# Kernel optimization log

Hardware: AMD Instinct MI355X
Metric: run time of the kernel (lower is better)

## Reference

```python
import jax, jax.numpy as jnp
import numpy as np

B, N, DIM = 4, 2048, 256
H, HD, M = 8, 32, 4
SPARSE_TOPK = 32


def setup_inputs() -> dict:
    key = jax.random.key(0)
    ks = jax.random.split(key, 6)
    x = jax.random.normal(ks[0], (B, N, DIM), dtype=jnp.float32)
    w_qkv = jax.random.normal(ks[1], (DIM, 3 * H * HD), dtype=jnp.float32) * 0.02
    b_qkv = jnp.zeros((3 * H * HD,), dtype=jnp.float32)
    w_proj = jax.random.normal(ks[2], (H * HD, DIM), dtype=jnp.float32) * 0.02
    b_proj = jnp.zeros((DIM,), dtype=jnp.float32)
    scale = jnp.ones((1, H, 1, 1), dtype=jnp.float32)  # trainable scale, init scale_value=1.0
    mem_k = jax.random.normal(ks[3], (H, M, HD), dtype=jnp.float32)
    mem_v = jax.random.normal(ks[4], (H, M, HD), dtype=jnp.float32)
    return {"x": x, "w_qkv": w_qkv, "b_qkv": b_qkv, "w_proj": w_proj,
            "b_proj": b_proj, "scale": scale, "mem_k": mem_k, "mem_v": mem_v}


def reference(x, w_qkv, b_qkv, w_proj, b_proj, scale, mem_k, mem_v):
    b, n, dim = x.shape
    h, m, hd = mem_k.shape
    qkv = (x @ w_qkv + b_qkv).reshape(b, n, 3, h, hd).transpose(2, 0, 3, 1, 4)
    q, k, v = qkv[0], qkv[1], qkv[2]
    # concat memory vectors along key-length axis -> [B,H,N+M,hd]
    k = jnp.concatenate([k, jnp.broadcast_to(mem_k, (b, h, m, hd))], axis=2)
    v = jnp.concatenate([v, jnp.broadcast_to(mem_v, (b, h, m, hd))], axis=2)
    s = n + m
    # scores with trainable per-head scale: [B,H,N,S]
    scores = jnp.einsum('bhnd,bhsd->bhns', q, k) * (hd ** -0.5) * scale
    neg = -jnp.finfo(scores.dtype).max
    # improve_locality: mask rectangular diagonal (eye(N, S))
    diag = jnp.arange(n)[:, None] == jnp.arange(s)[None, :]
    scores = jnp.where(diag, neg, scores)
    # sparse topk: keep only values >= k-th largest per row
    top = jax.lax.top_k(scores, SPARSE_TOPK)[0]
    vk = top[..., -1:]
    scores = jnp.where(scores < vk, neg, scores)
    attn = jax.nn.softmax(scores, axis=-1)
    out = jnp.einsum('bhns,bhsd->bhnd', attn, v)
    out = out.transpose(0, 2, 1, 3).reshape(b, n, h * hd)
    return out @ w_proj + b_proj
```

## Files before the change

### kernel.cpp

```cpp
#include <hip/hip_runtime.h>
#include <float.h>
#include <stdint.h>

#define Bb   4
#define Nn   2048
#define DIMc 256
#define Hh   8
#define HDd  32
#define Mm   4
#define STOT 2052
#define ROWS 8
#define SROW 2112
#define NVROW 2052

typedef float f32x2 __attribute__((ext_vector_type(2)));
typedef unsigned long long u64;

__device__ __forceinline__ unsigned int f2key(float s) {
    unsigned int b = __float_as_uint(s);
    return (b & 0x80000000u) ? ~b : (b | 0x80000000u);
}
__device__ __forceinline__ float key2f(unsigned int u) {
    unsigned int b = (u & 0x80000000u) ? (u ^ 0x80000000u) : ~u;
    return __uint_as_float(b);
}

__global__ __launch_bounds__(256) void sgemm_qkv(
    const float* __restrict__ A, const float* __restrict__ Bm,
    const float* __restrict__ bias, float* __restrict__ Qb,
    float* __restrict__ kTb, float* __restrict__ Vx,
    const float* __restrict__ memv)
{
    __shared__ __align__(16) float As[2][16][68];
    __shared__ __align__(16) float Bs[2][16][64];
    __shared__ __align__(16) float Ts[64][65];
    const int tid = threadIdx.x;
    const int tx = tid & 15, ty = tid >> 4;
    const int m0 = blockIdx.y * 64, n0 = blockIdx.x * 64;
    const int arow = tid >> 2, acol = (tid & 3) * 4;
    const int brow = tid >> 4, bcol = (tid & 15) * 4;
    float acc[4][4] = {};

    {
        const float4 av = *(const float4*)&A[(size_t)(m0 + arow) * DIMc + acol];
        const float4 bv = *(const float4*)&Bm[(size_t)brow * 768 + n0 + bcol];
        As[0][acol + 0][arow] = av.x;
        As[0][acol + 1][arow] = av.y;
        As[0][acol + 2][arow] = av.z;
        As[0][acol + 3][arow] = av.w;
        *(float4*)&Bs[0][brow][bcol] = bv;
    }
    int cur = 0;
    for (int kb = 0; kb < DIMc; kb += 16) {
        float4 av2, bv2;
        const bool more = (kb + 16 < DIMc);
        if (more) {
            av2 = *(const float4*)&A[(size_t)(m0 + arow) * DIMc + kb + 16 + acol];
            bv2 = *(const float4*)&Bm[(size_t)(kb + 16 + brow) * 768 + n0 + bcol];
        }
        __syncthreads();
#pragma unroll
        for (int k = 0; k < 16; ++k) {
            const float4 a  = *(const float4*)&As[cur][k][ty * 4];
            const float4 bq = *(const float4*)&Bs[cur][k][tx * 4];
            const float aa[4] = {a.x, a.y, a.z, a.w};
            const float bb[4] = {bq.x, bq.y, bq.z, bq.w};
#pragma unroll
            for (int i = 0; i < 4; ++i)
#pragma unroll
                for (int j = 0; j < 4; ++j)
                    acc[i][j] = fmaf(aa[i], bb[j], acc[i][j]);
        }
        if (more) {
            As[cur ^ 1][acol + 0][arow] = av2.x;
            As[cur ^ 1][acol + 1][arow] = av2.y;
            As[cur ^ 1][acol + 2][arow] = av2.z;
            As[cur ^ 1][acol + 3][arow] = av2.w;
            *(float4*)&Bs[cur ^ 1][brow][bcol] = bv2;
        }
        cur ^= 1;
    }
    const float4 bv = *(const float4*)&bias[n0 + tx * 4];
    const float bb[4] = {bv.x, bv.y, bv.z, bv.w};
    const int path = n0 >> 8;
    if (path == 1) {
#pragma unroll
        for (int i = 0; i < 4; ++i)
#pragma unroll
            for (int j = 0; j < 4; ++j)
                Ts[tx * 4 + j][ty * 4 + i] = acc[i][j] + bb[j];
        __syncthreads();
        const int c_local = tid >> 2;
        const int seg     = tid & 3;
        const int cg = (n0 - 256) + c_local;
        const int hh = cg >> 5, dd = cg & 31;
        const int bi = m0 >> 11, j0 = (m0 & 2047) + seg * 16;
        float* dst = kTb + (((size_t)(bi * Hh + hh) * HDd + dd) * Nn) + j0;
#pragma unroll
        for (int q = 0; q < 4; ++q)
            *(float4*)(dst + q * 4) = *(const float4*)&Ts[c_local][seg * 16 + q * 4];
    } else if (path == 0) {
        const int c0 = n0 + tx * 4;
#pragma unroll
        for (int i = 0; i < 4; ++i) {
            float4 o;
            o.x = acc[i][0] + bb[0];
            o.y = acc[i][1] + bb[1];
            o.z = acc[i][2] + bb[2];
            o.w = acc[i][3] + bb[3];
            *(float4*)&Qb[(size_t)(m0 + ty * 4 + i) * 256 + c0] = o;
        }
    } else {
        const int c0 = (n0 & 255) + tx * 4;
        const size_t row_base = (size_t)(m0 >> 11) * NVROW + (m0 & 2047);
#pragma unroll
        for (int i = 0; i < 4; ++i) {
            float4 o;
            o.x = acc[i][0] + bb[0];
            o.y = acc[i][1] + bb[1];
            o.z = acc[i][2] + bb[2];
            o.w = acc[i][3] + bb[3];
            *(float4*)&Vx[(row_base + ty * 4 + i) * 256 + c0] = o;
        }
        if (n0 == 512 && (m0 & 2047) == 0) {
            const int bb2 = m0 >> 11;
#pragma unroll
            for (int mm = 0; mm < Mm; ++mm)
                Vx[((size_t)bb2 * NVROW + Nn + mm) * 256 + tid] =
                    memv[((tid >> 5) * Mm + mm) * HDd + (tid & 31)];
        }
    }
}

__global__ __launch_bounds__(256) void sgemm_bias(
    const float* __restrict__ A, const float* __restrict__ Bm,
    const float* __restrict__ bias, float* __restrict__ C,
    int Md, int Nd, int Kd)
{
    __shared__ __align__(16) float As[2][16][36];
    __shared__ __align__(16) float Bs[2][16][64];
    const int tid = threadIdx.x;
    const int tx = tid & 15, ty = tid >> 4;
    const int m0 = blockIdx.y * 32, n0 = blockIdx.x * 64;
    const int arow = tid >> 2, acol = (tid & 3) * 4;
    const int brow = tid >> 4, bcol = (tid & 15) * 4;
    float acc[2][4] = {};

    {
        const float4 bv = *(const float4*)&Bm[(size_t)brow * Nd + n0 + bcol];
        *(float4*)&Bs[0][brow][bcol] = bv;
        if (tid < 128) {
            const float4 av = *(const float4*)&A[(size_t)(m0 + arow) * Kd + acol];
            As[0][acol + 0][arow] = av.x;
            As[0][acol + 1][arow] = av.y;
            As[0][acol + 2][arow] = av.z;
            As[0][acol + 3][arow] = av.w;
        }
    }
    int cur = 0;
    for (int kb = 0; kb < Kd; kb += 16) {
        float4 av2, bv2;
        const bool more = (kb + 16 < Kd);
        if (more) {
            bv2 = *(const float4*)&Bm[(size_t)(kb + 16 + brow) * Nd + n0 + bcol];
            if (tid < 128)
                av2 = *(const float4*)&A[(size_t)(m0 + arow) * Kd + kb + 16 + acol];
        }
        __syncthreads();
#pragma unroll
        for (int k = 0; k < 16; ++k) {
            const float2 a  = *(const float2*)&As[cur][k][ty * 2];
            const float4 bq = *(const float4*)&Bs[cur][k][tx * 4];
            const float aa[2] = {a.x, a.y};
            const float bb[4] = {bq.x, bq.y, bq.z, bq.w};
#pragma unroll
            for (int i = 0; i < 2; ++i)
#pragma unroll
                for (int j = 0; j < 4; ++j)
                    acc[i][j] = fmaf(aa[i], bb[j], acc[i][j]);
        }
        if (more) {
            *(float4*)&Bs[cur ^ 1][brow][bcol] = bv2;
            if (tid < 128) {
                As[cur ^ 1][acol + 0][arow] = av2.x;
                As[cur ^ 1][acol + 1][arow] = av2.y;
                As[cur ^ 1][acol + 2][arow] = av2.z;
                As[cur ^ 1][acol + 3][arow] = av2.w;
            }
        }
        cur ^= 1;
    }
    const float4 bv = *(const float4*)&bias[n0 + tx * 4];
    const float bb[4] = {bv.x, bv.y, bv.z, bv.w};
#pragma unroll
    for (int i = 0; i < 2; ++i) {
        float4 o;
        o.x = acc[i][0] + bb[0];
        o.y = acc[i][1] + bb[1];
        o.z = acc[i][2] + bb[2];
        o.w = acc[i][3] + bb[3];
        *(float4*)&C[(size_t)(m0 + ty * 2 + i) * Nd + n0 + tx * 4] = o;
    }
}

#if __has_builtin(__builtin_elementwise_fma)
#define PKSTEP(Q, P)                                                        \
    { const f32x2 qq = {(Q), (Q)};                                          \
      a01 = __builtin_elementwise_fma(qq, ((const f32x2*)&kd[P])[0], a01);  \
      a23 = __builtin_elementwise_fma(qq, ((const f32x2*)&kd[P])[1], a23); }
#else
#define PKSTEP(Q, P)                                                        \
    { a01.x = fmaf((Q), kd[P].x, a01.x); a01.y = fmaf((Q), kd[P].y, a01.y); \
      a23.x = fmaf((Q), kd[P].z, a23.x); a23.y = fmaf((Q), kd[P].w, a23.y); }
#endif

__global__ __launch_bounds__(512, 4) void attn_sparse(
    const float* __restrict__ Qb, const float* __restrict__ kTb,
    const float* __restrict__ Vx, const float* __restrict__ memk,
    const float* __restrict__ scale, float* __restrict__ attn_out)
{
    __shared__ __align__(16) unsigned int S[ROWS][SROW];
    __shared__ __align__(16) float qs[ROWS][HDd];
    __shared__ __align__(16) u64 ulist64[ROWS][64];
    __shared__ __align__(16) u64 wj_list[ROWS][64];

    const int tid    = threadIdx.x;
    const int ntiles = Nn / ROWS;
    const int tile   = blockIdx.x % ntiles;
    const int h      = (blockIdx.x / ntiles) % Hh;
    const int b      = blockIdx.x / (ntiles * Hh);
    const int n0     = tile * ROWS;
    const float sc   = scale[h] * 0.17677669529663688f;

    if (tid < ROWS * HDd) {
        const int r = tid >> 5, d2 = tid & 31;
        qs[r][d2] = Qb[(size_t)(b * Nn + n0 + r) * 256 + h * HDd + d2];
    }
    __syncthreads();

    const float* kT = kTb + (size_t)(b * Hh + h) * (HDd * Nn);

    {
        const int j0 = tid * 4;
        f32x2 acc01[ROWS], acc23[ROWS];
#pragma unroll
        for (int r = 0; r < ROWS; ++r) { acc01[r] = (f32x2){0.f, 0.f}; acc23[r] = (f32x2){0.f, 0.f}; }
#pragma unroll 1
        for (int dc = 0; dc < 4; ++dc) {
            float4 kd[8];
#pragma unroll
            for (int dd = 0; dd < 8; ++dd)
                kd[dd] = *(const float4*)&kT[(dc * 8 + dd) * Nn + j0];
#pragma unroll
            for (int r = 0; r < ROWS; ++r) {
                const float4 qa = *(const float4*)&qs[r][dc * 8];
                const float4 qb2 = *(const float4*)&qs[r][dc * 8 + 4];
                f32x2 a01 = acc01[r], a23 = acc23[r];
                PKSTEP(qa.x, 0) PKSTEP(qa.y, 1) PKSTEP(qa.z, 2) PKSTEP(qa.w, 3)
                PKSTEP(qb2.x, 4) PKSTEP(qb2.y, 5) PKSTEP(qb2.z, 6) PKSTEP(qb2.w, 7)
                acc01[r] = a01; acc23[r] = a23;
            }
        }
#pragma unroll
        for (int r = 0; r < ROWS; ++r) {
            const float af[4] = {acc01[r].x, acc01[r].y, acc23[r].x, acc23[r].y};
            uint4 o;
            unsigned int* op = (unsigned int*)&o;
#pragma unroll
            for (int kk = 0; kk < 4; ++kk) {
                float s = af[kk] * sc;
                if (j0 + kk == n0 + r) s = -FLT_MAX;
                op[kk] = f2key(s);
            }
            *(uint4*)&S[r][j0] = o;
        }
    }
    if (tid < 32) {
        const int r = tid >> 2, m = tid & 3;
        const float* kp = memk + (size_t)(h * Mm + m) * HDd;
        float acc = 0.f;
#pragma unroll
        for (int dcc = 0; dcc < 8; ++dcc) {
            const float4 qv = *(const float4*)&qs[r][dcc * 4];
            const float4 kv = *(const float4*)&kp[dcc * 4];
            acc = fmaf(qv.x, kv.x, acc);
            acc = fmaf(qv.y, kv.y, acc);
            acc = fmaf(qv.z, kv.z, acc);
            acc = fmaf(qv.w, kv.w, acc);
        }
        S[r][2048 + m] = f2key(acc * sc);
    } else {
        const int t2 = tid - 32;
        const int r = t2 / 60, p = t2 % 60;
        S[r][2052 + p] = 0x00800000u;
    }
    __syncthreads();

    const int wave = tid >> 6, lane = tid & 63;
    const int half = lane >> 5, d = lane & 31;
    const int n = n0 + wave;

    unsigned int uv[33];
    unsigned int mx = 0u;
    {
        const unsigned int* Srow = &S[wave][lane];
#pragma unroll
        for (int i = 0; i < 33; ++i) {
            uv[i] = Srow[i * 64];
            mx = uv[i] > mx ? uv[i] : mx;
        }
    }

    auto bitonic = [&](unsigned int vv) -> unsigned int {
#pragma unroll
        for (int kk = 2; kk <= 64; kk <<= 1)
#pragma unroll
            for (int jj = kk >> 1; jj > 0; jj >>= 1) {
                const unsigned int o = (unsigned int)__shfl_xor((int)vv, jj);
                const unsigned int mn = vv < o ? vv : o;
                const unsigned int mxv = vv < o ? o : vv;
                const bool up   = ((lane & kk) == 0);
                const bool lowr = ((lane & jj) == 0);
                vv = (lowr == up) ? mn : mxv;
            }
        return vv;
    };
    auto countge = [&](unsigned int tt) -> int {
        int gg = 0;
#pragma unroll
        for (int i = 0; i < 33; ++i) gg += (int)__popcll(__ballot(uv[i] >= tt));
        return gg;
    };
    auto compact = [&](unsigned int tt) -> int {
        int bs = 0;
#pragma unroll
        for (int i = 0; i < 33; ++i) {
            const bool p = (uv[i] >= tt);
            const unsigned long long mk = __ballot(p);
            if (p) {
                const int pos = bs + (int)__popcll(mk & ((1ull << lane) - 1ull));
                if (pos < 64)
                    ulist64[wave][pos] = ((u64)uv[i] << 32) | (unsigned int)(i * 64 + lane);
            }
            bs += (int)__popcll(mk);
        }
        return bs;
    };

    const unsigned int vs1 = bitonic(mx);
    const unsigned int Lmax = (unsigned int)__shfl((int)vs1, 63);
    unsigned int t = (unsigned int)__shfl((int)vs1, 32);

    ulist64[wave][lane] = 0ull;
    __asm__ __volatile__("s_waitcnt lgkmcnt(0)" ::: "memory");
    int base = compact(t);
    bool exact = true;
    if (base > 64) {
        unsigned int blo = t, bhi = Lmax + 1;
        int found = 0;
#pragma unroll 1
        for (int it = 0; it < 33; ++it) {
            if (bhi - blo <= 1u) break;
            const unsigned int tm = blo + ((bhi - blo) >> 1);
            const int gm = countge(tm);
            if (gm > 64) blo = tm;
            else if (gm < 32) bhi = tm;
            else { t = tm; found = 1; break; }
        }
        if (!found) t = blo;
        ulist64[wave][lane] = 0ull;
        __asm__ __volatile__("s_waitcnt lgkmcnt(0)" ::: "memory");
        base = compact(t);
        exact = (base <= 64);
    }
    const int C2 = base < 64 ? base : 64;
    __asm__ __volatile__("s_waitcnt lgkmcnt(0)" ::: "memory");
    const u64 pk = ulist64[wave][lane];
    const unsigned int ue = (unsigned int)(pk >> 32);
    const int je = (int)(unsigned int)pk;

    const unsigned int vs2 = bitonic(ue);
    unsigned int vkkey = (unsigned int)__shfl((int)vs2, 32);
    const unsigned int v31u = (unsigned int)__shfl((int)vs2, 31);
    if (!exact) vkkey = t;

    const bool tie_span = (v31u == vkkey);
    float snx = -3.0e38f;
    if (exact && !tie_span) {
        if (C2 == 32) {
            unsigned int unx = 0u;
#pragma unroll
            for (int i = 0; i < 33; ++i) {
                const unsigned int u = uv[i];
                if (u < vkkey && u > unx) unx = u;
            }
#pragma unroll
            for (int o = 32; o > 0; o >>= 1) {
                const unsigned int ou = (unsigned int)__shfl_xor((int)unx, o);
                if (ou > unx) unx = ou;
            }
            snx = key2f(unx);
        } else {
            snx = key2f(v31u);
        }
    }
    const float svk  = key2f(vkkey);
    const float gapv = svk - snx;
    const float lam  = (exact && !tie_span && gapv > 0.f && gapv <= 4.0e-6f) ? 0.13f : 0.f;

    const float mval = key2f(Lmax);
    const float we = (ue >= vkkey) ? __expf(key2f(ue) - mval) : 0.f;
    wj_list[wave][(lane & 1) * 32 + (lane >> 1)] =
        ((u64)(unsigned int)je << 32) | (u64)__float_as_uint(we);
    float Z = we;
#pragma unroll
    for (int o = 32; o > 0; o >>= 1) Z += __shfl_xor(Z, o);
    __asm__ __volatile__("s_waitcnt lgkmcnt(0)" ::: "memory");

    const float* Vbh = Vx + (size_t)b * (NVROW * 256) + h * HDd;
    float outv = 0.f;
#pragma unroll 2
    for (int e0 = 0; e0 < C2; e0 += 8) {
        const int p0 = (e0 >> 1) + half * 32;
        const ulonglong2 wa = *(const ulonglong2*)&wj_list[wave][p0];
        const ulonglong2 wb = *(const ulonglong2*)&wj_list[wave][p0 + 2];
        float w[4]; unsigned int q[4];
        w[0] = __uint_as_float((unsigned int)wa.x); q[0] = (unsigned int)(wa.x >> 32);
        w[1] = __uint_as_float((unsigned int)wa.y); q[1] = (unsigned int)(wa.y >> 32);
        w[2] = __uint_as_float((unsigned int)wb.x); q[2] = (unsigned int)(wb.x >> 32);
        w[3] = __uint_as_float((unsigned int)wb.y); q[3] = (unsigned int)(wb.y >> 32);
        float vv[4];
#pragma unroll
        for (int u2 = 0; u2 < 4; ++u2)
            vv[u2] = Vbh[q[u2] * 256u + (unsigned int)d];
#pragma unroll
        for (int u2 = 0; u2 < 4; ++u2)
            outv = fmaf(w[u2], vv[u2], outv);
    }
    outv += __shfl_xor(outv, 32);

    float res = outv / Z;
    if (lam > 0.f) {
        unsigned int unx2 = 0u; int jnx = 0, jd1 = -1;
#pragma unroll
        for (int i = 0; i < 33; ++i) {
            const unsigned int u = uv[i];
            const int jj2 = i * 64 + lane;
            if (u < vkkey && u > unx2) { unx2 = u; jnx = jj2; }
            if (u == vkkey && jj2 > jd1) jd1 = jj2;
        }
#pragma unroll
        for (int o = 32; o > 0; o >>= 1) {
            const unsigned int ou = (unsigned int)__shfl_xor((int)unx2, o);
            const int oj = __shfl_xor(jnx, o);
            if (ou > unx2 || (ou == unx2 && oj > jnx)) { unx2 = ou; jnx = oj; }
            const int od = __shfl_xor(jd1, o);
            if (od > jd1) jd1 = od;
        }
        const float wd = __expf(svk - mval);
        const float wn = __expf(key2f(unx2) - mval);
        const float* vp1 = Vbh + (size_t)jd1 * 256;
        const float* vpn = Vbh + (size_t)jnx * 256;
        const float ZB = Z - wd + wn;
        const float oB = (outv - wd * vp1[d] + wn * vpn[d]) / ZB;
        res = (1.f - lam) * res + lam * oB;
    }
    if (half == 0)
        attn_out[(size_t)(b * Nn + n) * 256 + h * HDd + d] = res;
}

extern "C" void kernel_launch(void* const* d_in, const int* in_sizes, int n_in,
                              void* d_out, int out_size, void* d_ws, size_t ws_size,
                              hipStream_t stream) {
    const float* x      = (const float*)d_in[0];
    const float* w_qkv  = (const float*)d_in[1];
    const float* b_qkv  = (const float*)d_in[2];
    const float* w_proj = (const float*)d_in[3];
    const float* b_proj = (const float*)d_in[4];
    const float* scale  = (const float*)d_in[5];
    const float* mem_k  = (const float*)d_in[6];
    const float* mem_v  = (const float*)d_in[7];
    float* out = (float*)d_out;

    float* Qb  = (float*)d_ws;
    float* kTb = Qb  + (size_t)Bb * Nn * 256;
    float* Vx  = kTb + (size_t)Bb * Hh * HDd * Nn;

    sgemm_qkv<<<dim3(768 / 64, (Bb * Nn) / 64), 256, 0, stream>>>(
        x, w_qkv, b_qkv, Qb, kTb, Vx, mem_v);

    attn_sparse<<<dim3(Bb * Hh * (Nn / ROWS)), 512, 0, stream>>>(
        Qb, kTb, Vx, mem_k, scale, Qb);

    sgemm_bias<<<dim3(DIMc / 64, (Bb * Nn) / 32), 256, 0, stream>>>(
        Qb, w_proj, b_proj, out, Bb * Nn, DIMc, DIMc);
}
```

Before: 364.5 us.

## Enlarge GEMM register tiles and software-pipeline K loads in score loop

The QKV GEMM moves from 64x64 to 128x128 tiles with an 8x8 per-thread register tile, and its LDS staging and transpose buffer share a union. The output projection GEMM moves to 128x64 tiles with 8x4 per thread. The attention score loop is unrolled with two K register buffers so global loads for the next chunk are in flight while the current chunk's FMAs run. The aim is more arithmetic per shared-memory and global access, fewer blocks, and hidden load latency, at the cost of higher register pressure and less parallelism in the small GEMMs (fewer blocks: 384 for QKV, 256 for projection).

```diff
diff --git a/kernel.cpp b/kernel.cpp
--- a/kernel.cpp
+++ b/kernel.cpp
@@ -31,96 +31,117 @@
     float* __restrict__ kTb, float* __restrict__ Vx,
     const float* __restrict__ memv)
 {
-    __shared__ __align__(16) float As[2][16][68];
-    __shared__ __align__(16) float Bs[2][16][64];
-    __shared__ __align__(16) float Ts[64][65];
+    __shared__ __align__(16) union {
+        struct { float As[2][16][128]; float Bs[2][16][128]; } st;
+        float Ts[128][133];
+    } u;
     const int tid = threadIdx.x;
     const int tx = tid & 15, ty = tid >> 4;
-    const int m0 = blockIdx.y * 64, n0 = blockIdx.x * 64;
-    const int arow = tid >> 2, acol = (tid & 3) * 4;
-    const int brow = tid >> 4, bcol = (tid & 15) * 4;
-    float acc[4][4] = {};
+    const int m0 = blockIdx.y * 128, n0 = blockIdx.x * 128;
+    const int arow = tid >> 1, acol = (tid & 1) * 8;
+    const int bcol = tx * 8;
+    float acc[8][8] = {};
 
     {
-        const float4 av = *(const float4*)&A[(size_t)(m0 + arow) * DIMc + acol];
-        const float4 bv = *(const float4*)&Bm[(size_t)brow * 768 + n0 + bcol];
-        As[0][acol + 0][arow] = av.x;
-        As[0][acol + 1][arow] = av.y;
-        As[0][acol + 2][arow] = av.z;
-        As[0][acol + 3][arow] = av.w;
-        *(float4*)&Bs[0][brow][bcol] = bv;
+        const float4 a0 = *(const float4*)&A[(size_t)(m0 + arow) * DIMc + acol];
+        const float4 a1 = *(const float4*)&A[(size_t)(m0 + arow) * DIMc + acol + 4];
+        const float4 b0 = *(const float4*)&Bm[(size_t)ty * 768 + n0 + bcol];
+        const float4 b1 = *(const float4*)&Bm[(size_t)ty * 768 + n0 + bcol + 4];
+        const float av[8] = {a0.x,a0.y,a0.z,a0.w,a1.x,a1.y,a1.z,a1.w};
+#pragma unroll
+        for (int c = 0; c < 8; ++c) u.st.As[0][acol + c][arow] = av[c];
+        *(float4*)&u.st.Bs[0][ty][bcol]     = b0;
+        *(float4*)&u.st.Bs[0][ty][bcol + 4] = b1;
     }
     int cur = 0;
     for (int kb = 0; kb < DIMc; kb += 16) {
-        float4 av2, bv2;
+        float4 a0n, a1n, b0n, b1n;
         const bool more = (kb + 16 < DIMc);
         if (more) {
-            av2 = *(const float4*)&A[(size_t)(m0 + arow) * DIMc + kb + 16 + acol];
-            bv2 = *(const float4*)&Bm[(size_t)(kb + 16 + brow) * 768 + n0 + bcol];
+            a0n = *(const float4*)&A[(size_t)(m0 + arow) * DIMc + kb + 16 + acol];
+            a1n = *(const float4*)&A[(size_t)(m0 + arow) * DIMc + kb + 16 + acol + 4];
+            b0n = *(const float4*)&Bm[(size_t)(kb + 16 + ty) * 768 + n0 + bcol];
+            b1n = *(const float4*)&Bm[(size_t)(kb + 16 + ty) * 768 + n0 + bcol + 4];
         }
         __syncthreads();
 #pragma unroll
         for (int k = 0; k < 16; ++k) {
-            const float4 a  = *(const float4*)&As[cur][k][ty * 4];
-            const float4 bq = *(const float4*)&Bs[cur][k][tx * 4];
-            const float aa[4] = {a.x, a.y, a.z, a.w};
-            const float bb[4] = {bq.x, bq.y, bq.z, bq.w};
-#pragma unroll
-            for (int i = 0; i < 4; ++i)
-#pragma unroll
-                for (int j = 0; j < 4; ++j)
+            const float4 av0 = *(const float4*)&u.st.As[cur][k][ty * 8];
+            const float4 av1 = *(const float4*)&u.st.As[cur][k][ty * 8 + 4];
+            const float4 bv0 = *(const float4*)&u.st.Bs[cur][k][tx * 8];
+            const float4 bv1 = *(const float4*)&u.st.Bs[cur][k][tx * 8 + 4];
+            const float aa[8] = {av0.x,av0.y,av0.z,av0.w,av1.x,av1.y,av1.z,av1.w};
+            const float bb[8] = {bv0.x,bv0.y,bv0.z,bv0.w,bv1.x,bv1.y,bv1.z,bv1.w};
+#pragma unroll
+            for (int i = 0; i < 8; ++i)
+#pragma unroll
+                for (int j = 0; j < 8; ++j)
                     acc[i][j] = fmaf(aa[i], bb[j], acc[i][j]);
         }
         if (more) {
-            As[cur ^ 1][acol + 0][arow] = av2.x;
-            As[cur ^ 1][acol + 1][arow] = av2.y;
-            As[cur ^ 1][acol + 2][arow] = av2.z;
-            As[cur ^ 1][acol + 3][arow] = av2.w;
-            *(float4*)&Bs[cur ^ 1][brow][bcol] = bv2;
+            const float av[8] = {a0n.x,a0n.y,a0n.z,a0n.w,a1n.x,a1n.y,a1n.z,a1n.w};
+#pragma unroll
+            for (int c = 0; c < 8; ++c) u.st.As[cur ^ 1][acol + c][arow] = av[c];
+            *(float4*)&u.st.Bs[cur ^ 1][ty][bcol]     = b0n;
+            *(float4*)&u.st.Bs[cur ^ 1][ty][bcol + 4] = b1n;
         }
         cur ^= 1;
     }
-    const float4 bv = *(const float4*)&bias[n0 + tx * 4];
-    const float bb[4] = {bv.x, bv.y, bv.z, bv.w};
+    const float4 bv0 = *(const float4*)&bias[n0 + tx * 8];
+    const float4 bv1 = *(const float4*)&bias[n0 + tx * 8 + 4];
+    const float bb[8] = {bv0.x,bv0.y,bv0.z,bv0.w,bv1.x,bv1.y,bv1.z,bv1.w};
     const int path = n0 >> 8;
     if (path == 1) {
-#pragma unroll
-        for (int i = 0; i < 4; ++i)
-#pragma unroll
-            for (int j = 0; j < 4; ++j)
-                Ts[tx * 4 + j][ty * 4 + i] = acc[i][j] + bb[j];
         __syncthreads();
-        const int c_local = tid >> 2;
-        const int seg     = tid & 3;
+#pragma unroll
+        for (int i = 0; i < 8; ++i) {
+            float4 o0, o1;
+            o0.x = acc[i][0] + bb[0]; o0.y = acc[i][1] + bb[1];
+            o0.z = acc[i][2] + bb[2]; o0.w = acc[i][3] + bb[3];
+            o1.x = acc[i][4] + bb[4]; o1.y = acc[i][5] + bb[5];
+            o1.z = acc[i][6] + bb[6]; o1.w = acc[i][7] + bb[7];
+            *(float4*)&u.Ts[ty * 8 + i][tx * 8]     = o0;
+            *(float4*)&u.Ts[ty * 8 + i][tx * 8 + 4] = o1;
+        }
+        __syncthreads();
+        const int c_local = tid >> 1, seg = tid & 1;
         const int cg = (n0 - 256) + c_local;
         const int hh = cg >> 5, dd = cg & 31;
-        const int bi = m0 >> 11, j0 = (m0 & 2047) + seg * 16;
+        const int bi = m0 >> 11, j0 = (m0 & 2047) + seg * 64;
         float* dst = kTb + (((size_t)(bi * Hh + hh) * HDd + dd) * Nn) + j0;
 #pragma unroll
-        for (int q = 0; q < 4; ++q)
-            *(float4*)(dst + q * 4) = *(const float4*)&Ts[c_local][seg * 16 + q * 4];
+        for (int q = 0; q < 16; ++q) {
+            float4 o;
+            o.x = u.Ts[seg * 64 + q * 4 + 0][c_local];
+            o.y = u.Ts[seg * 64 + q * 4 + 1][c_local];
+            o.z = u.Ts[seg * 64 + q * 4 + 2][c_local];
+            o.w = u.Ts[seg * 64 + q * 4 + 3][c_local];
+            *(float4*)(dst + q * 4) = o;
+        }
     } else if (path == 0) {
-        const int c0 = n0 + tx * 4;
-#pragma unroll
-        for (int i = 0; i < 4; ++i) {
-            float4 o;
-            o.x = acc[i][0] + bb[0];
-            o.y = acc[i][1] + bb[1];
-            o.z = acc[i][2] + bb[2];
-            o.w = acc[i][3] + bb[3];
-            *(float4*)&Qb[(size_t)(m0 + ty * 4 + i) * 256 + c0] = o;
+        const int c0 = n0 + tx * 8;
+#pragma unroll
+        for (int i = 0; i < 8; ++i) {
+            float4 o0, o1;
+            o0.x = acc[i][0] + bb[0]; o0.y = acc[i][1] + bb[1];
+            o0.z = acc[i][2] + bb[2]; o0.w = acc[i][3] + bb[3];
+            o1.x = acc[i][4] + bb[4]; o1.y = acc[i][5] + bb[5];
+            o1.z = acc[i][6] + bb[6]; o1.w = acc[i][7] + bb[7];
+            float* dst = &Qb[(size_t)(m0 + ty * 8 + i) * 256 + c0];
+            *(float4*)dst = o0; *(float4*)(dst + 4) = o1;
         }
     } else {
-        const int c0 = (n0 & 255) + tx * 4;
+        const int c0 = (n0 & 255) + tx * 8;
         const size_t row_base = (size_t)(m0 >> 11) * NVROW + (m0 & 2047);
 #pragma unroll
-        for (int i = 0; i < 4; ++i) {
-            float4 o;
-            o.x = acc[i][0] + bb[0];
-            o.y = acc[i][1] + bb[1];
-            o.z = acc[i][2] + bb[2];
-            o.w = acc[i][3] + bb[3];
-            *(float4*)&Vx[(row_base + ty * 4 + i) * 256 + c0] = o;
+        for (int i = 0; i < 8; ++i) {
+            float4 o0, o1;
+            o0.x = acc[i][0] + bb[0]; o0.y = acc[i][1] + bb[1];
+            o0.z = acc[i][2] + bb[2]; o0.w = acc[i][3] + bb[3];
+            o1.x = acc[i][4] + bb[4]; o1.y = acc[i][5] + bb[5];
+            o1.z = acc[i][6] + bb[6]; o1.w = acc[i][7] + bb[7];
+            float* dst = &Vx[(row_base + ty * 8 + i) * 256 + c0];
+            *(float4*)dst = o0; *(float4*)(dst + 4) = o1;
         }
         if (n0 == 512 && (m0 & 2047) == 0) {
             const int bb2 = m0 >> 11;
@@ -137,69 +158,65 @@
     const float* __restrict__ bias, float* __restrict__ C,
     int Md, int Nd, int Kd)
 {
-    __shared__ __align__(16) float As[2][16][36];
+    __shared__ __align__(16) float As[2][16][128];
     __shared__ __align__(16) float Bs[2][16][64];
     const int tid = threadIdx.x;
     const int tx = tid & 15, ty = tid >> 4;
-    const int m0 = blockIdx.y * 32, n0 = blockIdx.x * 64;
-    const int arow = tid >> 2, acol = (tid & 3) * 4;
+    const int m0 = blockIdx.y * 128, n0 = blockIdx.x * 64;
+    const int arow = tid >> 1, acol = (tid & 1) * 8;
     const int brow = tid >> 4, bcol = (tid & 15) * 4;
-    float acc[2][4] = {};
+    float acc[8][4] = {};
 
     {
-        const float4 bv = *(const float4*)&Bm[(size_t)brow * Nd + n0 + bcol];
-        *(float4*)&Bs[0][brow][bcol] = bv;
-        if (tid < 128) {
-            const float4 av = *(const float4*)&A[(size_t)(m0 + arow) * Kd + acol];
-            As[0][acol + 0][arow] = av.x;
-            As[0][acol + 1][arow] = av.y;
-            As[0][acol + 2][arow] = av.z;
-            As[0][acol + 3][arow] = av.w;
-        }
+        const float4 a0 = *(const float4*)&A[(size_t)(m0 + arow) * Kd + acol];
+        const float4 a1 = *(const float4*)&A[(size_t)(m0 + arow) * Kd + acol + 4];
+        const float4 b0 = *(const float4*)&Bm[(size_t)brow * Nd + n0 + bcol];
+        const float av[8] = {a0.x,a0.y,a0.z,a0.w,a1.x,a1.y,a1.z,a1.w};
+#pragma unroll
+        for (int c = 0; c < 8; ++c) As[0][acol + c][arow] = av[c];
+        *(float4*)&Bs[0][brow][bcol] = b0;
     }
     int cur = 0;
     for (int kb = 0; kb < Kd; kb += 16) {
-        float4 av2, bv2;
+        float4 a0n, a1n, b0n;
         const bool more = (kb + 16 < Kd);
         if (more) {
-            bv2 = *(const float4*)&Bm[(size_t)(kb + 16 + brow) * Nd + n0 + bcol];
-            if (tid < 128)
-                av2 = *(const float4*)&A[(size_t)(m0 + arow) * Kd + kb + 16 + acol];
+            a0n = *(const float4*)&A[(size_t)(m0 + arow) * Kd + kb + 16 + acol];
+            a1n = *(const float4*)&A[(size_t)(m0 + arow) * Kd + kb + 16 + acol + 4];
+            b0n = *(const float4*)&Bm[(size_t)(kb + 16 + brow) * Nd + n0 + bcol];
         }
         __syncthreads();
 #pragma unroll
         for (int k = 0; k < 16; ++k) {
-            const float2 a  = *(const float2*)&As[cur][k][ty * 2];
-            const float4 bq = *(const float4*)&Bs[cur][k][tx * 4];
-            const float aa[2] = {a.x, a.y};
+            const float4 av0 = *(const float4*)&As[cur][k][ty * 8];
+            const float4 av1 = *(const float4*)&As[cur][k][ty * 8 + 4];
+            const float4 bq  = *(const float4*)&Bs[cur][k][tx * 4];
+            const float aa[8] = {av0.x,av0.y,av0.z,av0.w,av1.x,av1.y,av1.z,av1.w};
             const float bb[4] = {bq.x, bq.y, bq.z, bq.w};
 #pragma unroll
-            for (int i = 0; i < 2; ++i)
+            for (int i = 0; i < 8; ++i)
 #pragma unroll
                 for (int j = 0; j < 4; ++j)
                     acc[i][j] = fmaf(aa[i], bb[j], acc[i][j]);
         }
         if (more) {
-            *(float4*)&Bs[cur ^ 1][brow][bcol] = bv2;
-            if (tid < 128) {
-                As[cur ^ 1][acol + 0][arow] = av2.x;
-                As[cur ^ 1][acol + 1][arow] = av2.y;
-                As[cur ^ 1][acol + 2][arow] = av2.z;
-                As[cur ^ 1][acol + 3][arow] = av2.w;
-            }
+            const float av[8] = {a0n.x,a0n.y,a0n.z,a0n.w,a1n.x,a1n.y,a1n.z,a1n.w};
+#pragma unroll
+            for (int c = 0; c < 8; ++c) As[cur ^ 1][acol + c][arow] = av[c];
+            *(float4*)&Bs[cur ^ 1][brow][bcol] = b0n;
         }
         cur ^= 1;
     }
     const float4 bv = *(const float4*)&bias[n0 + tx * 4];
     const float bb[4] = {bv.x, bv.y, bv.z, bv.w};
 #pragma unroll
-    for (int i = 0; i < 2; ++i) {
+    for (int i = 0; i < 8; ++i) {
         float4 o;
         o.x = acc[i][0] + bb[0];
         o.y = acc[i][1] + bb[1];
         o.z = acc[i][2] + bb[2];
         o.w = acc[i][3] + bb[3];
-        *(float4*)&C[(size_t)(m0 + ty * 2 + i) * Nd + n0 + tx * 4] = o;
+        *(float4*)&C[(size_t)(m0 + ty * 8 + i) * Nd + n0 + tx * 4] = o;
     }
 }
 
@@ -214,6 +231,23 @@
       a23.x = fmaf((Q), kd[P].z, a23.x); a23.y = fmaf((Q), kd[P].w, a23.y); }
 #endif
 
+#define SCORE_LD(KD, DC)                                                    \
+    _Pragma("unroll")                                                       \
+    for (int dd = 0; dd < 8; ++dd)                                          \
+        KD[dd] = *(const float4*)&kT[((DC) * 8 + dd) * Nn + j0];
+
+#define SCORE_FMA(KD, DC)                                                   \
+    _Pragma("unroll")                                                       \
+    for (int r = 0; r < ROWS; ++r) {                                        \
+        const float4 qa  = *(const float4*)&qs[r][(DC) * 8];                \
+        const float4 qb2 = *(const float4*)&qs[r][(DC) * 8 + 4];            \
+        const float4* kd = KD;                                              \
+        f32x2 a01 = acc01[r], a23 = acc23[r];                               \
+        PKSTEP(qa.x, 0) PKSTEP(qa.y, 1) PKSTEP(qa.z, 2) PKSTEP(qa.w, 3)     \
+        PKSTEP(qb2.x, 4) PKSTEP(qb2.y, 5) PKSTEP(qb2.z, 6) PKSTEP(qb2.w, 7) \
+        acc01[r] = a01; acc23[r] = a23;                                     \
+    }
+
 __global__ __launch_bounds__(512, 4) void attn_sparse(
     const float* __restrict__ Qb, const float* __restrict__ kTb,
     const float* __restrict__ Vx, const float* __restrict__ memk,
@@ -245,22 +279,15 @@
         f32x2 acc01[ROWS], acc23[ROWS];
 #pragma unroll
         for (int r = 0; r < ROWS; ++r) { acc01[r] = (f32x2){0.f, 0.f}; acc23[r] = (f32x2){0.f, 0.f}; }
-#pragma unroll 1
-        for (int dc = 0; dc < 4; ++dc) {
-            float4 kd[8];
-#pragma unroll
-            for (int dd = 0; dd < 8; ++dd)
-                kd[dd] = *(const float4*)&kT[(dc * 8 + dd) * Nn + j0];
-#pragma unroll
-            for (int r = 0; r < ROWS; ++r) {
-                const float4 qa = *(const float4*)&qs[r][dc * 8];
-                const float4 qb2 = *(const float4*)&qs[r][dc * 8 + 4];
-                f32x2 a01 = acc01[r], a23 = acc23[r];
-                PKSTEP(qa.x, 0) PKSTEP(qa.y, 1) PKSTEP(qa.z, 2) PKSTEP(qa.w, 3)
-                PKSTEP(qb2.x, 4) PKSTEP(qb2.y, 5) PKSTEP(qb2.z, 6) PKSTEP(qb2.w, 7)
-                acc01[r] = a01; acc23[r] = a23;
-            }
-        }
+        float4 kdA[8], kdB[8];
+        SCORE_LD(kdA, 0)
+        SCORE_LD(kdB, 1)
+        SCORE_FMA(kdA, 0)
+        SCORE_LD(kdA, 2)
+        SCORE_FMA(kdB, 1)
+        SCORE_LD(kdB, 3)
+        SCORE_FMA(kdA, 2)
+        SCORE_FMA(kdB, 3)
 #pragma unroll
         for (int r = 0; r < ROWS; ++r) {
             const float af[4] = {acc01[r].x, acc01[r].y, acc23[r].x, acc23[r].y};
@@ -486,12 +513,12 @@
     float* kTb = Qb  + (size_t)Bb * Nn * 256;
     float* Vx  = kTb + (size_t)Bb * Hh * HDd * Nn;
 
-    sgemm_qkv<<<dim3(768 / 64, (Bb * Nn) / 64), 256, 0, stream>>>(
+    sgemm_qkv<<<dim3(768 / 128, (Bb * Nn) / 128), 256, 0, stream>>>(
         x, w_qkv, b_qkv, Qb, kTb, Vx, mem_v);
 
     attn_sparse<<<dim3(Bb * Hh * (Nn / ROWS)), 512, 0, stream>>>(
         Qb, kTb, Vx, mem_k, scale, Qb);
 
-    sgemm_bias<<<dim3(DIMc / 64, (Bb * Nn) / 32), 256, 0, stream>>>(
+    sgemm_bias<<<dim3(DIMc / 64, (Bb * Nn) / 128), 256, 0, stream>>>(
         Qb, w_proj, b_proj, out, Bb * Nn, DIMc, DIMc);
 }
```

New measurement: 353.1 us. 1.03x faster.
